# Performance work log

Hardware: AMD Instinct MI355X
Metric: run time of the kernel (lower is better)

## Reference

```python
import jax, jax.numpy as jnp
import numpy as np

N_QUBITS = 4
DIM = 2 ** N_QUBITS  # 16 statevector amplitudes


def _cnot_perm(c, t):
    # CNOT(control=c, target=t) is a permutation of basis states (its own inverse).
    # wire 0 is the most-significant bit (default.qubit convention).
    perm = np.arange(DIM)
    for k in range(DIM):
        if (k >> (N_QUBITS - 1 - c)) & 1:
            perm[k] = k ^ (1 << (N_QUBITS - 1 - t))
    return perm

CNOT_PERMS = [jnp.asarray(_cnot_perm(q, (q + 1) % N_QUBITS)) for q in range(N_QUBITS)]
# Z_SIGNS[q, k] = +1 if qubit q is |0> in basis state k else -1
Z_SIGNS = jnp.asarray(
    np.array([[1.0 - 2.0 * ((k >> (N_QUBITS - 1 - q)) & 1) for k in range(DIM)]
              for q in range(N_QUBITS)], dtype=np.float32))


def _apply_rx(state, theta, q):
    # state: (N, 16) complex64; theta: scalar or (N,); q: wire index
    n = state.shape[0]
    st = state.reshape(n, 2 ** q, 2, 2 ** (N_QUBITS - 1 - q))
    a0, a1 = st[:, :, 0, :], st[:, :, 1, :]
    c = jnp.reshape(jnp.cos(theta * 0.5), (-1, 1, 1))
    s = jnp.reshape(jnp.sin(theta * 0.5), (-1, 1, 1))
    new0 = c * a0 - 1j * s * a1
    new1 = c * a1 - 1j * s * a0
    return jnp.stack([new0, new1], axis=2).reshape(n, DIM)


def _quantum(angles, params):
    # angles: (N, 4) float32 input rotations; params: (4,) learned rotations
    n = angles.shape[0]
    state = jnp.zeros((n, DIM), jnp.complex64).at[:, 0].set(1.0)
    for q in range(N_QUBITS):
        state = _apply_rx(state, angles[:, q], q)
    for q in range(N_QUBITS):
        state = _apply_rx(state, params[q], q)
        state = state[:, CNOT_PERMS[q]]  # CNOT(q, (q+1)%4)
    probs = state.real ** 2 + state.imag ** 2  # (N, 16)
    return probs @ Z_SIGNS.T  # (N, 4) expvals of PauliZ


def setup_inputs() -> dict:
    key = jax.random.key(0)
    kx, kwi, kbi, kwo, kbo, kp = jax.random.split(key, 6)
    B, S, D = 16, 2048, 1024
    lim_i = 1.0 / np.sqrt(D)
    lim_o = 1.0 / np.sqrt(N_QUBITS)
    return {
        "x": jax.random.normal(kx, (B, S, D), jnp.float32),
        "Wi": jax.random.uniform(kwi, (D, N_QUBITS), jnp.float32, -lim_i, lim_i),
        "bi": jax.random.uniform(kbi, (N_QUBITS,), jnp.float32, -lim_i, lim_i),
        "Wo": jax.random.uniform(kwo, (N_QUBITS, D), jnp.float32, -lim_o, lim_o),
        "bo": jax.random.uniform(kbo, (D,), jnp.float32, -lim_o, lim_o),
        "ffn_params": jax.random.normal(kp, (N_QUBITS,), jnp.float32) * 0.1,
    }


def reference(x, Wi, bi, Wo, bo, ffn_params):
    B, S, D = x.shape
    xp = x @ Wi + bi                                  # (B, S, 4)
    mn = xp.min(axis=-1, keepdims=True)
    mx = xp.max(axis=-1, keepdims=True)
    ang = (xp - mn) / (mx - mn + 1e-8) * jnp.pi       # per-token min-max scale to [0, pi]
    q = _quantum(ang.reshape(-1, N_QUBITS), ffn_params).reshape(B, S, N_QUBITS)
    return q @ Wo + bo                                # (B, S, D); dropout = identity (eval)
```

## Files before the change

### kernel.cpp

```cpp
#include <hip/hip_runtime.h>

#define NQ      4
#define DIMQ    16
#define D_MODEL 1024
#define TPB     64
#define PI_F    3.14159265358979323846f

__global__ __launch_bounds__(256, 4)
void qffn_kernel(const float* __restrict__ x,
                 const float* __restrict__ Wi,
                 const float* __restrict__ bi,
                 const float* __restrict__ Wo,
                 const float* __restrict__ bo,
                 const float* __restrict__ fp,
                 float* __restrict__ out,
                 int n_tokens)
{
    __shared__ float s_xp[TPB * 4];
    __shared__ float s_q[TPB * 4];

    const int tid  = threadIdx.x;
    const int lane = tid & 63;
    const int w    = tid >> 6;
    const int tile = blockIdx.x * TPB;

    const float4* x4  = (const float4*)x;
    const float4* Wi4 = (const float4*)Wi;

    float4 wi[4][4];
    #pragma unroll
    for (int c = 0; c < 4; ++c) {
        #pragma unroll
        for (int e = 0; e < 4; ++e)
            wi[c][e] = Wi4[(c * 64 + lane) * 4 + e];
    }
    const float bi0 = bi[0], bi1 = bi[1], bi2 = bi[2], bi3 = bi[3];

    float k0 = 0.f, k1 = 0.f, k2 = 0.f, k3 = 0.f;

    #define DOT4(xe, wv) \
        p0 = fmaf(xe, wv.x, p0); p1 = fmaf(xe, wv.y, p1); \
        p2 = fmaf(xe, wv.z, p2); p3 = fmaf(xe, wv.w, p3);

    #pragma unroll 2
    for (int t = 0; t < 16; ++t) {
        int tok = tile + w * 16 + t;
        if (tok > n_tokens - 1) tok = n_tokens - 1;
        const size_t base = (size_t)tok * 256;
        float4 xv0 = x4[base + 0 * 64 + lane];
        float4 xv1 = x4[base + 1 * 64 + lane];
        float4 xv2 = x4[base + 2 * 64 + lane];
        float4 xv3 = x4[base + 3 * 64 + lane];

        float p0 = 0.f, p1 = 0.f, p2 = 0.f, p3 = 0.f;
        DOT4(xv0.x, wi[0][0]) DOT4(xv0.y, wi[0][1]) DOT4(xv0.z, wi[0][2]) DOT4(xv0.w, wi[0][3])
        DOT4(xv1.x, wi[1][0]) DOT4(xv1.y, wi[1][1]) DOT4(xv1.z, wi[1][2]) DOT4(xv1.w, wi[1][3])
        DOT4(xv2.x, wi[2][0]) DOT4(xv2.y, wi[2][1]) DOT4(xv2.z, wi[2][2]) DOT4(xv2.w, wi[2][3])
        DOT4(xv3.x, wi[3][0]) DOT4(xv3.y, wi[3][1]) DOT4(xv3.z, wi[3][2]) DOT4(xv3.w, wi[3][3])

        #pragma unroll
        for (int m = 1; m < 64; m <<= 1) {
            p0 += __shfl_xor(p0, m, 64);
            p1 += __shfl_xor(p1, m, 64);
            p2 += __shfl_xor(p2, m, 64);
            p3 += __shfl_xor(p3, m, 64);
        }
        if (lane == t) { k0 = p0; k1 = p1; k2 = p2; k3 = p3; }
    }

    if (lane < 16) {
        *(float4*)&s_xp[(w * 16 + lane) * 4] =
            make_float4(k0 + bi0, k1 + bi1, k2 + bi2, k3 + bi3);
    }

    const float4* Wo4 = (const float4*)Wo;
    const float4 wo0 = Wo4[0 * 256 + tid];
    const float4 wo1 = Wo4[1 * 256 + tid];
    const float4 wo2 = Wo4[2 * 256 + tid];
    const float4 wo3 = Wo4[3 * 256 + tid];
    const float4 bo4 = ((const float4*)bo)[tid];

    __syncthreads();

    if (tid < 64) {
        float4 xpv = *(const float4*)&s_xp[tid * 4];
        float xp0 = xpv.x, xp1 = xpv.y, xp2 = xpv.z, xp3 = xpv.w;

        float pc[NQ], ps[NQ];
        #pragma unroll
        for (int q = 0; q < NQ; ++q) {
            float h = 0.5f * fp[q];
            pc[q] = __cosf(h);
            ps[q] = __sinf(h);
        }

        float mn = fminf(fminf(xp0, xp1), fminf(xp2, xp3));
        float mx = fmaxf(fmaxf(xp0, xp1), fmaxf(xp2, xp3));
        float inv = PI_F / (mx - mn + 1e-8f);
        float ang[NQ];
        ang[0] = (xp0 - mn) * inv;
        ang[1] = (xp1 - mn) * inv;
        ang[2] = (xp2 - mn) * inv;
        ang[3] = (xp3 - mn) * inv;

        float sr[DIMQ], si[DIMQ];
        #pragma unroll
        for (int k = 0; k < DIMQ; ++k) { sr[k] = (k == 0) ? 1.0f : 0.0f; si[k] = 0.0f; }

        #pragma unroll
        for (int q = 0; q < NQ; ++q) {
            const int bit = 8 >> q;
            float h = 0.5f * ang[q];
            float cth = __cosf(h), sth = __sinf(h);
            #pragma unroll
            for (int k = 0; k < DIMQ; ++k) {
                if (!(k & bit)) {
                    const int k1 = k | bit;
                    float a0r = sr[k],  a0i = si[k];
                    float a1r = sr[k1], a1i = si[k1];
                    sr[k]  = fmaf(cth, a0r,  sth * a1i);
                    si[k]  = fmaf(cth, a0i, -sth * a1r);
                    sr[k1] = fmaf(cth, a1r,  sth * a0i);
                    si[k1] = fmaf(cth, a1i, -sth * a0r);
                }
            }
        }
        #pragma unroll
        for (int q = 0; q < NQ; ++q) {
            const int bit = 8 >> q;
            float cth = pc[q], sth = ps[q];
            #pragma unroll
            for (int k = 0; k < DIMQ; ++k) {
                if (!(k & bit)) {
                    const int k1 = k | bit;
                    float a0r = sr[k],  a0i = si[k];
                    float a1r = sr[k1], a1i = si[k1];
                    sr[k]  = fmaf(cth, a0r,  sth * a1i);
                    si[k]  = fmaf(cth, a0i, -sth * a1r);
                    sr[k1] = fmaf(cth, a1r,  sth * a0i);
                    si[k1] = fmaf(cth, a1i, -sth * a0r);
                }
            }
            const int cbit = 8 >> q;
            const int tbit = 8 >> ((q + 1) & 3);
            #pragma unroll
            for (int k = 0; k < DIMQ; ++k) {
                if ((k & cbit) && !(k & tbit)) {
                    const int k1 = k | tbit;
                    float t;
                    t = sr[k]; sr[k] = sr[k1]; sr[k1] = t;
                    t = si[k]; si[k] = si[k1]; si[k1] = t;
                }
            }
        }

        float pr[DIMQ];
        #pragma unroll
        for (int k = 0; k < DIMQ; ++k) pr[k] = fmaf(sr[k], sr[k], si[k] * si[k]);

        float qv0 = 0.f, qv1 = 0.f, qv2 = 0.f, qv3 = 0.f;
        #pragma unroll
        for (int k = 0; k < DIMQ; ++k) {
            qv0 += (k & 8) ? -pr[k] : pr[k];
            qv1 += (k & 4) ? -pr[k] : pr[k];
            qv2 += (k & 2) ? -pr[k] : pr[k];
            qv3 += (k & 1) ? -pr[k] : pr[k];
        }
        *(float4*)&s_q[tid * 4] = make_float4(qv0, qv1, qv2, qv3);
    }

    __syncthreads();

    float4* out4 = (float4*)out;
    #pragma unroll 8
    for (int i = 0; i < TPB; ++i) {
        int grow = tile + i;
        if (grow < n_tokens) {
            float4 qq = *(const float4*)&s_q[i * 4];
            float4 v;
            v.x = fmaf(qq.x, wo0.x, fmaf(qq.y, wo1.x, fmaf(qq.z, wo2.x, fmaf(qq.w, wo3.x, bo4.x))));
            v.y = fmaf(qq.x, wo0.y, fmaf(qq.y, wo1.y, fmaf(qq.z, wo2.y, fmaf(qq.w, wo3.y, bo4.y))));
            v.z = fmaf(qq.x, wo0.z, fmaf(qq.y, wo1.z, fmaf(qq.z, wo2.z, fmaf(qq.w, wo3.z, bo4.z))));
            v.w = fmaf(qq.x, wo0.w, fmaf(qq.y, wo1.w, fmaf(qq.z, wo2.w, fmaf(qq.w, wo3.w, bo4.w))));
            out4[(size_t)grow * 256 + tid] = v;
        }
    }
}

extern "C" void kernel_launch(void* const* d_in, const int* in_sizes, int n_in,
                              void* d_out, int out_size, void* d_ws, size_t ws_size,
                              hipStream_t stream)
{
    (void)d_ws; (void)ws_size; (void)n_in; (void)out_size;
    const float* x  = (const float*)d_in[0];
    const float* Wi = (const float*)d_in[1];
    const float* bi = (const float*)d_in[2];
    const float* Wo = (const float*)d_in[3];
    const float* bo = (const float*)d_in[4];
    const float* fp = (const float*)d_in[5];
    float* out = (float*)d_out;

    int n_tokens = in_sizes[0] / D_MODEL;
    int grid = (n_tokens + TPB - 1) / TPB;
    qffn_kernel<<<grid, 256, 0, stream>>>(x, Wi, bi, Wo, bo, fp, out, n_tokens);
}
```

Measured before the change: 242.5 us.

## Split input projection across waves by feature slice with shared-memory partial reduction

Each wave now processes all 64 tokens of the tile over a quarter of the feature dimension instead of 16 full tokens, and the four wave partials are summed through shared memory. This cuts per-thread weight registers and loads Wo before the loop. In exchange, each wave performs four times as many cross-lane shuffle reductions, and each token load per lane is a single float4.

```diff
diff --git a/kernel.cpp b/kernel.cpp
--- a/kernel.cpp
+++ b/kernel.cpp
@@ -16,7 +16,7 @@
                  float* __restrict__ out,
                  int n_tokens)
 {
-    __shared__ float s_xp[TPB * 4];
+    __shared__ float s_part[256 * 4];
     __shared__ float s_q[TPB * 4];
 
     const int tid  = threadIdx.x;
@@ -27,36 +27,31 @@
     const float4* x4  = (const float4*)x;
     const float4* Wi4 = (const float4*)Wi;
 
-    float4 wi[4][4];
-    #pragma unroll
-    for (int c = 0; c < 4; ++c) {
-        #pragma unroll
-        for (int e = 0; e < 4; ++e)
-            wi[c][e] = Wi4[(c * 64 + lane) * 4 + e];
-    }
-    const float bi0 = bi[0], bi1 = bi[1], bi2 = bi[2], bi3 = bi[3];
+    const float4 wiA = Wi4[tid * 4 + 0];
+    const float4 wiB = Wi4[tid * 4 + 1];
+    const float4 wiC = Wi4[tid * 4 + 2];
+    const float4 wiD = Wi4[tid * 4 + 3];
 
-    float k0 = 0.f, k1 = 0.f, k2 = 0.f, k3 = 0.f;
+    const float4* Wo4 = (const float4*)Wo;
+    const float4 wo0 = Wo4[0 * 256 + tid];
+    const float4 wo1 = Wo4[1 * 256 + tid];
+    const float4 wo2 = Wo4[2 * 256 + tid];
+    const float4 wo3 = Wo4[3 * 256 + tid];
+    const float4 bo4 = ((const float4*)bo)[tid];
 
-    #define DOT4(xe, wv) \
-        p0 = fmaf(xe, wv.x, p0); p1 = fmaf(xe, wv.y, p1); \
-        p2 = fmaf(xe, wv.z, p2); p3 = fmaf(xe, wv.w, p3);
+    float4 k = make_float4(0.f, 0.f, 0.f, 0.f);
 
-    #pragma unroll 2
-    for (int t = 0; t < 16; ++t) {
-        int tok = tile + w * 16 + t;
-        if (tok > n_tokens - 1) tok = n_tokens - 1;
-        const size_t base = (size_t)tok * 256;
-        float4 xv0 = x4[base + 0 * 64 + lane];
-        float4 xv1 = x4[base + 1 * 64 + lane];
-        float4 xv2 = x4[base + 2 * 64 + lane];
-        float4 xv3 = x4[base + 3 * 64 + lane];
+    const int last = n_tokens - 1;
+    #pragma unroll 8
+    for (int t = 0; t < TPB; ++t) {
+        int tok = tile + t; if (tok > last) tok = last;
+        float4 xv = x4[(size_t)tok * 256 + tid];
 
-        float p0 = 0.f, p1 = 0.f, p2 = 0.f, p3 = 0.f;
-        DOT4(xv0.x, wi[0][0]) DOT4(xv0.y, wi[0][1]) DOT4(xv0.z, wi[0][2]) DOT4(xv0.w, wi[0][3])
-        DOT4(xv1.x, wi[1][0]) DOT4(xv1.y, wi[1][1]) DOT4(xv1.z, wi[1][2]) DOT4(xv1.w, wi[1][3])
-        DOT4(xv2.x, wi[2][0]) DOT4(xv2.y, wi[2][1]) DOT4(xv2.z, wi[2][2]) DOT4(xv2.w, wi[2][3])
-        DOT4(xv3.x, wi[3][0]) DOT4(xv3.y, wi[3][1]) DOT4(xv3.z, wi[3][2]) DOT4(xv3.w, wi[3][3])
+        float p0, p1, p2, p3;
+        p0 = xv.x * wiA.x; p1 = xv.x * wiA.y; p2 = xv.x * wiA.z; p3 = xv.x * wiA.w;
+        p0 = fmaf(xv.y, wiB.x, p0); p1 = fmaf(xv.y, wiB.y, p1); p2 = fmaf(xv.y, wiB.z, p2); p3 = fmaf(xv.y, wiB.w, p3);
+        p0 = fmaf(xv.z, wiC.x, p0); p1 = fmaf(xv.z, wiC.y, p1); p2 = fmaf(xv.z, wiC.z, p2); p3 = fmaf(xv.z, wiC.w, p3);
+        p0 = fmaf(xv.w, wiD.x, p0); p1 = fmaf(xv.w, wiD.y, p1); p2 = fmaf(xv.w, wiD.z, p2); p3 = fmaf(xv.w, wiD.w, p3);
 
         #pragma unroll
         for (int m = 1; m < 64; m <<= 1) {
@@ -65,26 +60,21 @@
             p2 += __shfl_xor(p2, m, 64);
             p3 += __shfl_xor(p3, m, 64);
         }
-        if (lane == t) { k0 = p0; k1 = p1; k2 = p2; k3 = p3; }
+        if (lane == t) { k.x = p0; k.y = p1; k.z = p2; k.w = p3; }
     }
 
-    if (lane < 16) {
-        *(float4*)&s_xp[(w * 16 + lane) * 4] =
-            make_float4(k0 + bi0, k1 + bi1, k2 + bi2, k3 + bi3);
-    }
-
-    const float4* Wo4 = (const float4*)Wo;
-    const float4 wo0 = Wo4[0 * 256 + tid];
-    const float4 wo1 = Wo4[1 * 256 + tid];
-    const float4 wo2 = Wo4[2 * 256 + tid];
-    const float4 wo3 = Wo4[3 * 256 + tid];
-    const float4 bo4 = ((const float4*)bo)[tid];
-
+    *(float4*)&s_part[tid * 4] = k;
     __syncthreads();
 
     if (tid < 64) {
-        float4 xpv = *(const float4*)&s_xp[tid * 4];
-        float xp0 = xpv.x, xp1 = xpv.y, xp2 = xpv.z, xp3 = xpv.w;
+        float4 a0 = *(const float4*)&s_part[(0 * 64 + tid) * 4];
+        float4 a1 = *(const float4*)&s_part[(1 * 64 + tid) * 4];
+        float4 a2 = *(const float4*)&s_part[(2 * 64 + tid) * 4];
+        float4 a3 = *(const float4*)&s_part[(3 * 64 + tid) * 4];
+        float xp0 = a0.x + a1.x + a2.x + a3.x + bi[0];
+        float xp1 = a0.y + a1.y + a2.y + a3.y + bi[1];
+        float xp2 = a0.z + a1.z + a2.z + a3.z + bi[2];
+        float xp3 = a0.w + a1.w + a2.w + a3.w + bi[3];
 
         float pc[NQ], ps[NQ];
         #pragma unroll
@@ -105,7 +95,7 @@
 
         float sr[DIMQ], si[DIMQ];
         #pragma unroll
-        for (int k = 0; k < DIMQ; ++k) { sr[k] = (k == 0) ? 1.0f : 0.0f; si[k] = 0.0f; }
+        for (int kk = 0; kk < DIMQ; ++kk) { sr[kk] = (kk == 0) ? 1.0f : 0.0f; si[kk] = 0.0f; }
 
         #pragma unroll
         for (int q = 0; q < NQ; ++q) {
@@ -113,13 +103,13 @@
             float h = 0.5f * ang[q];
             float cth = __cosf(h), sth = __sinf(h);
             #pragma unroll
-            for (int k = 0; k < DIMQ; ++k) {
-                if (!(k & bit)) {
-                    const int k1 = k | bit;
-                    float a0r = sr[k],  a0i = si[k];
+            for (int kk = 0; kk < DIMQ; ++kk) {
+                if (!(kk & bit)) {
+                    const int k1 = kk | bit;
+                    float a0r = sr[kk], a0i = si[kk];
                     float a1r = sr[k1], a1i = si[k1];
-                    sr[k]  = fmaf(cth, a0r,  sth * a1i);
-                    si[k]  = fmaf(cth, a0i, -sth * a1r);
+                    sr[kk] = fmaf(cth, a0r,  sth * a1i);
+                    si[kk] = fmaf(cth, a0i, -sth * a1r);
                     sr[k1] = fmaf(cth, a1r,  sth * a0i);
                     si[k1] = fmaf(cth, a1i, -sth * a0r);
                 }
@@ -130,13 +120,13 @@
             const int bit = 8 >> q;
             float cth = pc[q], sth = ps[q];
             #pragma unroll
-            for (int k = 0; k < DIMQ; ++k) {
-                if (!(k & bit)) {
-                    const int k1 = k | bit;
-                    float a0r = sr[k],  a0i = si[k];
+            for (int kk = 0; kk < DIMQ; ++kk) {
+                if (!(kk & bit)) {
+                    const int k1 = kk | bit;
+                    float a0r = sr[kk], a0i = si[kk];
                     float a1r = sr[k1], a1i = si[k1];
-                    sr[k]  = fmaf(cth, a0r,  sth * a1i);
-                    si[k]  = fmaf(cth, a0i, -sth * a1r);
+                    sr[kk] = fmaf(cth, a0r,  sth * a1i);
+                    si[kk] = fmaf(cth, a0i, -sth * a1r);
                     sr[k1] = fmaf(cth, a1r,  sth * a0i);
                     si[k1] = fmaf(cth, a1i, -sth * a0r);
                 }
@@ -144,27 +134,27 @@
             const int cbit = 8 >> q;
             const int tbit = 8 >> ((q + 1) & 3);
             #pragma unroll
-            for (int k = 0; k < DIMQ; ++k) {
-                if ((k & cbit) && !(k & tbit)) {
-                    const int k1 = k | tbit;
-                    float t;
-                    t = sr[k]; sr[k] = sr[k1]; sr[k1] = t;
-                    t = si[k]; si[k] = si[k1]; si[k1] = t;
+            for (int kk = 0; kk < DIMQ; ++kk) {
+                if ((kk & cbit) && !(kk & tbit)) {
+                    const int k1 = kk | tbit;
+                    float tswap;
+                    tswap = sr[kk]; sr[kk] = sr[k1]; sr[k1] = tswap;
+                    tswap = si[kk]; si[kk] = si[k1]; si[k1] = tswap;
                 }
             }
         }
 
         float pr[DIMQ];
         #pragma unroll
-        for (int k = 0; k < DIMQ; ++k) pr[k] = fmaf(sr[k], sr[k], si[k] * si[k]);
+        for (int kk = 0; kk < DIMQ; ++kk) pr[kk] = fmaf(sr[kk], sr[kk], si[kk] * si[kk]);
 
         float qv0 = 0.f, qv1 = 0.f, qv2 = 0.f, qv3 = 0.f;
         #pragma unroll
-        for (int k = 0; k < DIMQ; ++k) {
-            qv0 += (k & 8) ? -pr[k] : pr[k];
-            qv1 += (k & 4) ? -pr[k] : pr[k];
-            qv2 += (k & 2) ? -pr[k] : pr[k];
-            qv3 += (k & 1) ? -pr[k] : pr[k];
+        for (int kk = 0; kk < DIMQ; ++kk) {
+            qv0 += (kk & 8) ? -pr[kk] : pr[kk];
+            qv1 += (kk & 4) ? -pr[kk] : pr[kk];
+            qv2 += (kk & 2) ? -pr[kk] : pr[kk];
+            qv3 += (kk & 1) ? -pr[kk] : pr[kk];
         }
         *(float4*)&s_q[tid * 4] = make_float4(qv0, qv1, qv2, qv3);
     }
```

New measurement: 242.4 us. Within noise of the previous version (-0.0%).

## Assign one token per 16-lane group and drop shared-memory staging

Applied to the files above, without the earlier changes.

Restructures the kernel so each 16-lane group handles one token end to end: a strided dot product with a 4-step shuffle reduction, the quantum simulation done redundantly in all 16 lanes, and the output row written directly. This removes both __syncthreads barriers and the serial phase where only 64 threads simulated circuits while the rest idled. Tiles shrink from 64 to 16 tokens per block, so the grid grows. Wi, Wo and bo are now re-read from global or cache inside the loops instead of being held in registers, and output writes are 16-lane segments instead of full-wave rows.

```diff
diff --git a/kernel.cpp b/kernel.cpp
--- a/kernel.cpp
+++ b/kernel.cpp
@@ -3,7 +3,7 @@
 #define NQ      4
 #define DIMQ    16
 #define D_MODEL 1024
-#define TPB     64
+#define TPB     16
 #define PI_F    3.14159265358979323846f
 
 __global__ __launch_bounds__(256, 4)
@@ -16,174 +16,145 @@
                  float* __restrict__ out,
                  int n_tokens)
 {
-    __shared__ float s_xp[TPB * 4];
-    __shared__ float s_q[TPB * 4];
-
     const int tid  = threadIdx.x;
     const int lane = tid & 63;
     const int w    = tid >> 6;
-    const int tile = blockIdx.x * TPB;
+    const int j    = lane & 15;
+    const int g    = lane >> 4;
+
+    int tok = blockIdx.x * TPB + w * 4 + g;
+    const int last = n_tokens - 1;
+    if (tok > last) tok = last;
 
     const float4* x4  = (const float4*)x;
     const float4* Wi4 = (const float4*)Wi;
+    const size_t  xbase = (size_t)tok * 256;
 
-    float4 wi[4][4];
-    #pragma unroll
-    for (int c = 0; c < 4; ++c) {
-        #pragma unroll
-        for (int e = 0; e < 4; ++e)
-            wi[c][e] = Wi4[(c * 64 + lane) * 4 + e];
-    }
-    const float bi0 = bi[0], bi1 = bi[1], bi2 = bi[2], bi3 = bi[3];
-
-    float k0 = 0.f, k1 = 0.f, k2 = 0.f, k3 = 0.f;
-
-    #define DOT4(xe, wv) \
-        p0 = fmaf(xe, wv.x, p0); p1 = fmaf(xe, wv.y, p1); \
-        p2 = fmaf(xe, wv.z, p2); p3 = fmaf(xe, wv.w, p3);
-
-    #pragma unroll 2
-    for (int t = 0; t < 16; ++t) {
-        int tok = tile + w * 16 + t;
-        if (tok > n_tokens - 1) tok = n_tokens - 1;
-        const size_t base = (size_t)tok * 256;
-        float4 xv0 = x4[base + 0 * 64 + lane];
-        float4 xv1 = x4[base + 1 * 64 + lane];
-        float4 xv2 = x4[base + 2 * 64 + lane];
-        float4 xv3 = x4[base + 3 * 64 + lane];
-
-        float p0 = 0.f, p1 = 0.f, p2 = 0.f, p3 = 0.f;
-        DOT4(xv0.x, wi[0][0]) DOT4(xv0.y, wi[0][1]) DOT4(xv0.z, wi[0][2]) DOT4(xv0.w, wi[0][3])
-        DOT4(xv1.x, wi[1][0]) DOT4(xv1.y, wi[1][1]) DOT4(xv1.z, wi[1][2]) DOT4(xv1.w, wi[1][3])
-        DOT4(xv2.x, wi[2][0]) DOT4(xv2.y, wi[2][1]) DOT4(xv2.z, wi[2][2]) DOT4(xv2.w, wi[2][3])
-        DOT4(xv3.x, wi[3][0]) DOT4(xv3.y, wi[3][1]) DOT4(xv3.z, wi[3][2]) DOT4(xv3.w, wi[3][3])
-
-        #pragma unroll
-        for (int m = 1; m < 64; m <<= 1) {
-            p0 += __shfl_xor(p0, m, 64);
-            p1 += __shfl_xor(p1, m, 64);
-            p2 += __shfl_xor(p2, m, 64);
-            p3 += __shfl_xor(p3, m, 64);
-        }
-        if (lane == t) { k0 = p0; k1 = p1; k2 = p2; k3 = p3; }
+    float p0 = 0.f, p1 = 0.f, p2 = 0.f, p3 = 0.f;
+    #pragma unroll 4
+    for (int i = 0; i < 16; ++i) {
+        const int s = i * 16 + j;
+        float4 xv = x4[xbase + s];
+        const float4* wr = Wi4 + ((size_t)s << 2);
+        float4 w0 = wr[0], w1 = wr[1], w2 = wr[2], w3 = wr[3];
+        p0 = fmaf(xv.x, w0.x, p0); p1 = fmaf(xv.x, w0.y, p1); p2 = fmaf(xv.x, w0.z, p2); p3 = fmaf(xv.x, w0.w, p3);
+        p0 = fmaf(xv.y, w1.x, p0); p1 = fmaf(xv.y, w1.y, p1); p2 = fmaf(xv.y, w1.z, p2); p3 = fmaf(xv.y, w1.w, p3);
+        p0 = fmaf(xv.z, w2.x, p0); p1 = fmaf(xv.z, w2.y, p1); p2 = fmaf(xv.z, w2.z, p2); p3 = fmaf(xv.z, w2.w, p3);
+        p0 = fmaf(xv.w, w3.x, p0); p1 = fmaf(xv.w, w3.y, p1); p2 = fmaf(xv.w, w3.z, p2); p3 = fmaf(xv.w, w3.w, p3);
     }
 
-    if (lane < 16) {
-        *(float4*)&s_xp[(w * 16 + lane) * 4] =
-            make_float4(k0 + bi0, k1 + bi1, k2 + bi2, k3 + bi3);
+    #pragma unroll
+    for (int m = 1; m < 16; m <<= 1) {
+        p0 += __shfl_xor(p0, m, 64);
+        p1 += __shfl_xor(p1, m, 64);
+        p2 += __shfl_xor(p2, m, 64);
+        p3 += __shfl_xor(p3, m, 64);
+    }
+
+    const float xp0 = p0 + bi[0];
+    const float xp1 = p1 + bi[1];
+    const float xp2 = p2 + bi[2];
+    const float xp3 = p3 + bi[3];
+
+    float mn = fminf(fminf(xp0, xp1), fminf(xp2, xp3));
+    float mx = fmaxf(fmaxf(xp0, xp1), fmaxf(xp2, xp3));
+    float inv = PI_F / (mx - mn + 1e-8f);
+    float ang[NQ];
+    ang[0] = (xp0 - mn) * inv;
+    ang[1] = (xp1 - mn) * inv;
+    ang[2] = (xp2 - mn) * inv;
+    ang[3] = (xp3 - mn) * inv;
+
+    float pc[NQ], ps[NQ];
+    #pragma unroll
+    for (int q = 0; q < NQ; ++q) {
+        float h = 0.5f * fp[q];
+        pc[q] = __cosf(h);
+        ps[q] = __sinf(h);
+    }
+
+    float sr[DIMQ], si[DIMQ];
+    #pragma unroll
+    for (int k = 0; k < DIMQ; ++k) { sr[k] = (k == 0) ? 1.0f : 0.0f; si[k] = 0.0f; }
+
+    #pragma unroll
+    for (int q = 0; q < NQ; ++q) {
+        const int bit = 8 >> q;
+        float h = 0.5f * ang[q];
+        float cth = __cosf(h), sth = __sinf(h);
+        #pragma unroll
+        for (int k = 0; k < DIMQ; ++k) {
+            if (!(k & bit)) {
+                const int k1 = k | bit;
+                float a0r = sr[k],  a0i = si[k];
+                float a1r = sr[k1], a1i = si[k1];
+                sr[k]  = fmaf(cth, a0r,  sth * a1i);
+                si[k]  = fmaf(cth, a0i, -sth * a1r);
+                sr[k1] = fmaf(cth, a1r,  sth * a0i);
+                si[k1] = fmaf(cth, a1i, -sth * a0r);
+            }
+        }
+    }
+    #pragma unroll
+    for (int q = 0; q < NQ; ++q) {
+        const int bit = 8 >> q;
+        float cth = pc[q], sth = ps[q];
+        #pragma unroll
+        for (int k = 0; k < DIMQ; ++k) {
+            if (!(k & bit)) {
+                const int k1 = k | bit;
+                float a0r = sr[k],  a0i = si[k];
+                float a1r = sr[k1], a1i = si[k1];
+                sr[k]  = fmaf(cth, a0r,  sth * a1i);
+                si[k]  = fmaf(cth, a0i, -sth * a1r);
+                sr[k1] = fmaf(cth, a1r,  sth * a0i);
+                si[k1] = fmaf(cth, a1i, -sth * a0r);
+            }
+        }
+        const int cbit = 8 >> q;
+        const int tbit = 8 >> ((q + 1) & 3);
+        #pragma unroll
+        for (int k = 0; k < DIMQ; ++k) {
+            if ((k & cbit) && !(k & tbit)) {
+                const int k1 = k | tbit;
+                float t;
+                t = sr[k]; sr[k] = sr[k1]; sr[k1] = t;
+                t = si[k]; si[k] = si[k1]; si[k1] = t;
+            }
+        }
+    }
+
+    float pr[DIMQ];
+    #pragma unroll
+    for (int k = 0; k < DIMQ; ++k) pr[k] = fmaf(sr[k], sr[k], si[k] * si[k]);
+
+    float qv0 = 0.f, qv1 = 0.f, qv2 = 0.f, qv3 = 0.f;
+    #pragma unroll
+    for (int k = 0; k < DIMQ; ++k) {
+        qv0 += (k & 8) ? -pr[k] : pr[k];
+        qv1 += (k & 4) ? -pr[k] : pr[k];
+        qv2 += (k & 2) ? -pr[k] : pr[k];
+        qv3 += (k & 1) ? -pr[k] : pr[k];
     }
 
     const float4* Wo4 = (const float4*)Wo;
-    const float4 wo0 = Wo4[0 * 256 + tid];
-    const float4 wo1 = Wo4[1 * 256 + tid];
-    const float4 wo2 = Wo4[2 * 256 + tid];
-    const float4 wo3 = Wo4[3 * 256 + tid];
-    const float4 bo4 = ((const float4*)bo)[tid];
+    const float4* bo4 = (const float4*)bo;
+    float4* out4 = (float4*)out;
 
-    __syncthreads();
-
-    if (tid < 64) {
-        float4 xpv = *(const float4*)&s_xp[tid * 4];
-        float xp0 = xpv.x, xp1 = xpv.y, xp2 = xpv.z, xp3 = xpv.w;
-
-        float pc[NQ], ps[NQ];
-        #pragma unroll
-        for (int q = 0; q < NQ; ++q) {
-            float h = 0.5f * fp[q];
-            pc[q] = __cosf(h);
-            ps[q] = __sinf(h);
-        }
-
-        float mn = fminf(fminf(xp0, xp1), fminf(xp2, xp3));
-        float mx = fmaxf(fmaxf(xp0, xp1), fmaxf(xp2, xp3));
-        float inv = PI_F / (mx - mn + 1e-8f);
-        float ang[NQ];
-        ang[0] = (xp0 - mn) * inv;
-        ang[1] = (xp1 - mn) * inv;
-        ang[2] = (xp2 - mn) * inv;
-        ang[3] = (xp3 - mn) * inv;
-
-        float sr[DIMQ], si[DIMQ];
-        #pragma unroll
-        for (int k = 0; k < DIMQ; ++k) { sr[k] = (k == 0) ? 1.0f : 0.0f; si[k] = 0.0f; }
-
-        #pragma unroll
-        for (int q = 0; q < NQ; ++q) {
-            const int bit = 8 >> q;
-            float h = 0.5f * ang[q];
-            float cth = __cosf(h), sth = __sinf(h);
-            #pragma unroll
-            for (int k = 0; k < DIMQ; ++k) {
-                if (!(k & bit)) {
-                    const int k1 = k | bit;
-                    float a0r = sr[k],  a0i = si[k];
-                    float a1r = sr[k1], a1i = si[k1];
-                    sr[k]  = fmaf(cth, a0r,  sth * a1i);
-                    si[k]  = fmaf(cth, a0i, -sth * a1r);
-                    sr[k1] = fmaf(cth, a1r,  sth * a0i);
-                    si[k1] = fmaf(cth, a1i, -sth * a0r);
-                }
-            }
-        }
-        #pragma unroll
-        for (int q = 0; q < NQ; ++q) {
-            const int bit = 8 >> q;
-            float cth = pc[q], sth = ps[q];
-            #pragma unroll
-            for (int k = 0; k < DIMQ; ++k) {
-                if (!(k & bit)) {
-                    const int k1 = k | bit;
-                    float a0r = sr[k],  a0i = si[k];
-                    float a1r = sr[k1], a1i = si[k1];
-                    sr[k]  = fmaf(cth, a0r,  sth * a1i);
-                    si[k]  = fmaf(cth, a0i, -sth * a1r);
-                    sr[k1] = fmaf(cth, a1r,  sth * a0i);
-                    si[k1] = fmaf(cth, a1i, -sth * a0r);
-                }
-            }
-            const int cbit = 8 >> q;
-            const int tbit = 8 >> ((q + 1) & 3);
-            #pragma unroll
-            for (int k = 0; k < DIMQ; ++k) {
-                if ((k & cbit) && !(k & tbit)) {
-                    const int k1 = k | tbit;
-                    float t;
-                    t = sr[k]; sr[k] = sr[k1]; sr[k1] = t;
-                    t = si[k]; si[k] = si[k1]; si[k1] = t;
-                }
-            }
-        }
-
-        float pr[DIMQ];
-        #pragma unroll
-        for (int k = 0; k < DIMQ; ++k) pr[k] = fmaf(sr[k], sr[k], si[k] * si[k]);
-
-        float qv0 = 0.f, qv1 = 0.f, qv2 = 0.f, qv3 = 0.f;
-        #pragma unroll
-        for (int k = 0; k < DIMQ; ++k) {
-            qv0 += (k & 8) ? -pr[k] : pr[k];
-            qv1 += (k & 4) ? -pr[k] : pr[k];
-            qv2 += (k & 2) ? -pr[k] : pr[k];
-            qv3 += (k & 1) ? -pr[k] : pr[k];
-        }
-        *(float4*)&s_q[tid * 4] = make_float4(qv0, qv1, qv2, qv3);
-    }
-
-    __syncthreads();
-
-    float4* out4 = (float4*)out;
-    #pragma unroll 8
-    for (int i = 0; i < TPB; ++i) {
-        int grow = tile + i;
-        if (grow < n_tokens) {
-            float4 qq = *(const float4*)&s_q[i * 4];
-            float4 v;
-            v.x = fmaf(qq.x, wo0.x, fmaf(qq.y, wo1.x, fmaf(qq.z, wo2.x, fmaf(qq.w, wo3.x, bo4.x))));
-            v.y = fmaf(qq.x, wo0.y, fmaf(qq.y, wo1.y, fmaf(qq.z, wo2.y, fmaf(qq.w, wo3.y, bo4.y))));
-            v.z = fmaf(qq.x, wo0.z, fmaf(qq.y, wo1.z, fmaf(qq.z, wo2.z, fmaf(qq.w, wo3.z, bo4.z))));
-            v.w = fmaf(qq.x, wo0.w, fmaf(qq.y, wo1.w, fmaf(qq.z, wo2.w, fmaf(qq.w, wo3.w, bo4.w))));
-            out4[(size_t)grow * 256 + tid] = v;
-        }
+    #pragma unroll 4
+    for (int i = 0; i < 16; ++i) {
+        const int c = i * 16 + j;
+        float4 wa = Wo4[0 * 256 + c];
+        float4 wb = Wo4[1 * 256 + c];
+        float4 wc = Wo4[2 * 256 + c];
+        float4 wd = Wo4[3 * 256 + c];
+        float4 bb = bo4[c];
+        float4 v;
+        v.x = fmaf(qv0, wa.x, fmaf(qv1, wb.x, fmaf(qv2, wc.x, fmaf(qv3, wd.x, bb.x))));
+        v.y = fmaf(qv0, wa.y, fmaf(qv1, wb.y, fmaf(qv2, wc.y, fmaf(qv3, wd.y, bb.y))));
+        v.z = fmaf(qv0, wa.z, fmaf(qv1, wb.z, fmaf(qv2, wc.z, fmaf(qv3, wd.z, bb.z))));
+        v.w = fmaf(qv0, wa.w, fmaf(qv1, wb.w, fmaf(qv2, wc.w, fmaf(qv3, wd.w, bb.w))));
+        out4[xbase + c] = v;
     }
 }
 
```

New measurement: 272.1 us. 1.12x slower.
